# Optimization experiments

Hardware: AMD Instinct MI355X
Metric: run time of the kernel (lower is better)

The kernel has to match this reference:

```python
import jax, jax.numpy as jnp
import numpy as np

EMBED = 1152
HEADS = 16
HEAD_DIM = EMBED // HEADS
SCALE = HEAD_DIM ** -0.5


def setup_inputs() -> dict:
    key = jax.random.key(0)
    k1, k2, k3, k4, k5 = jax.random.split(key, 5)
    B, S = 32, 729
    std = EMBED ** -0.5
    return {
        "hidden_state": jax.random.normal(k1, (B, S, EMBED), dtype=jnp.float32),
        "qkv_w": jax.random.normal(k2, (3 * EMBED, EMBED), dtype=jnp.float32) * std,
        "qkv_b": jax.random.normal(k3, (3 * EMBED,), dtype=jnp.float32) * 0.02,
        "out_w": jax.random.normal(k4, (EMBED, EMBED), dtype=jnp.float32) * std,
        "out_b": jax.random.normal(k5, (EMBED,), dtype=jnp.float32) * 0.02,
    }


def reference(hidden_state, qkv_w, qkv_b, out_w, out_b):
    B, S, _ = hidden_state.shape
    qkv = hidden_state @ qkv_w.T + qkv_b  # [B,S,3E]
    q, k, v = jnp.split(qkv, 3, axis=-1)
    # [B,S,E] -> [B,H,S,Dh]
    def heads(x):
        return x.reshape(B, S, HEADS, HEAD_DIM).transpose(0, 2, 1, 3)
    q, k, v = heads(q), heads(k), heads(v)
    scores = jnp.einsum("bhqd,bhkd->bhqk", q, k) * SCALE
    scores = jax.nn.softmax(scores, axis=-1)  # [B,H,S,S]
    out = jnp.einsum("bhqk,bhkd->bhqd", scores, v)
    out = out.transpose(0, 2, 1, 3).reshape(B, S, EMBED)
    out = out @ out_w.T + out_b
    return out, scores
```

## Files before the change

### kernel.cpp

```cpp
#include <hip/hip_runtime.h>

#define B_    32
#define S_    729
#define E_    1152
#define H_    16
#define D_    72
#define M1_   23328
#define MPAD_ 23424
#define SQ_   736
#define SK_   768
#define DP_   96
#define VR_   96
#define SCALE_ 0.11785113019775793f

typedef __attribute__((ext_vector_type(8))) _Float16 f16x8;
typedef __attribute__((ext_vector_type(4))) _Float16 f16x4;
typedef __attribute__((ext_vector_type(4))) float    f32x4;

#define GLDS16(g, l) __builtin_amdgcn_global_load_lds(                      \
    (__attribute__((address_space(1))) void*)(g),                           \
    (__attribute__((address_space(3))) void*)(l), 16, 0, 0)

union H2U { _Float16 h[2]; uint32_t u; };

#define N4H  6718464
#define N4W1 995328
#define N4W2 331776
#define NQC  (512 * 736 * 3)
#define NKC  (512 * 768 * 3)
#define NVR  (512 * 72)
__global__ void cvt_all(const float* __restrict__ hid, const float* __restrict__ w1,
                        const float* __restrict__ w2, _Float16* __restrict__ o1,
                        _Float16* __restrict__ o2, _Float16* __restrict__ o3,
                        _Float16* __restrict__ Qp, _Float16* __restrict__ Kp,
                        _Float16* __restrict__ Vtp) {
  const int stride = gridDim.x * blockDim.x;
  const int tid0 = blockIdx.x * blockDim.x + threadIdx.x;
  const uint4 z4 = make_uint4(0, 0, 0, 0);
  for (int idx = tid0; idx < NQC; idx += stride) {
    int row = idx / 3, c = idx - row * 3;
    *(uint4*)((char*)Qp + (size_t)row * 192 + 144 + c * 16) = z4;
  }
  for (int idx = tid0; idx < NKC; idx += stride) {
    int row = idx / 3, c = idx - row * 3;
    *(uint4*)((char*)Kp + (size_t)row * 192 + 144 + c * 16) = z4;
  }
  for (int idx = tid0; idx < NVR; idx += stride) {
    _Float16* p = Vtp + (size_t)idx * 768 + 729;
    #pragma unroll
    for (int s = 0; s < 39; ++s) p[s] = (_Float16)0.0f;
  }
  for (int i = tid0; i < N4H + N4W1 + N4W2; i += stride) {
    const float* s; _Float16* d; int j;
    if (i < N4H)             { s = hid; d = o1; j = i; }
    else if (i < N4H + N4W1) { s = w1;  d = o2; j = i - N4H; }
    else                     { s = w2;  d = o3; j = i - N4H - N4W1; }
    f32x4 v = __builtin_nontemporal_load((const f32x4*)(s + (size_t)j * 4));
    f16x4 o;
    o[0] = (_Float16)v[0]; o[1] = (_Float16)v[1];
    o[2] = (_Float16)v[2]; o[3] = (_Float16)v[3];
    __builtin_nontemporal_store(o, (f16x4*)(d + (size_t)j * 4));
  }
}

template<int MODE>
__global__ __launch_bounds__(256)
void gemm_f16(const _Float16* __restrict__ A, const _Float16* __restrict__ W,
              const float* __restrict__ bias,
              _Float16* __restrict__ Qp, _Float16* __restrict__ Kp,
              _Float16* __restrict__ Vtp, float* __restrict__ Cout)
{
  int mb, nb;
  if (MODE == 0) {
    const int xcd  = blockIdx.x & 7;
    const int slot = blockIdx.x >> 3;
    const int st   = slot >> 4;
    const int w    = slot & 15;
    const int stm  = st % 6, stn = st / 6;
    const int mloc = stm * 4 + (w & 3);
    nb = stn * 4 + (w >> 2);
    const int stripe = (xcd < 7) ? 23 : 22;
    if (mloc >= stripe || nb >= 27) return;
    mb = (xcd < 7 ? xcd * 23 : 161) + mloc;
  } else {
    mb = blockIdx.x; nb = blockIdx.y;
  }

  __shared__ _Float16 As[128 * 64];
  __shared__ _Float16 Bs[128 * 64];
  const int tid = threadIdx.x;
  const int l  = tid & 63;
  const int wv = tid >> 6;
  const int lq = l & 15, lk = l >> 4;
  const int m0 = mb * 128;
  const int n0 = nb * 128;
  const int wm = (wv & 1) * 64, wn = (wv >> 1) * 64;
  const int srow = l >> 3;
  const int scol = (l & 7) * 8;

  f32x4 acc[4][4] = {};

  for (int k0 = 0; k0 < 1152; k0 += 64) {
    #pragma unroll
    for (int q = 0; q < 4; ++q) {
      int chunk = wv * 4 + q;
      int row = chunk * 8 + srow;
      GLDS16(A + (size_t)(m0 + row) * 1152 + k0 + scol, &As[chunk * 512 + l * 8]);
      GLDS16(W + (size_t)(n0 + row) * 1152 + k0 + scol, &Bs[chunk * 512 + l * 8]);
    }
    __syncthreads();
    #pragma unroll
    for (int kk = 0; kk < 64; kk += 32) {
      f16x8 a[4], b[4];
      #pragma unroll
      for (int i = 0; i < 4; ++i)
        a[i] = *(const f16x8*)&As[(wm + 16 * i + lq) * 64 + kk + lk * 8];
      #pragma unroll
      for (int j = 0; j < 4; ++j)
        b[j] = *(const f16x8*)&Bs[(wn + 16 * j + lq) * 64 + kk + lk * 8];
      #pragma unroll
      for (int i = 0; i < 4; ++i)
        #pragma unroll
        for (int j = 0; j < 4; ++j)
          acc[i][j] = __builtin_amdgcn_mfma_f32_16x16x32_f16(a[i], b[j], acc[i][j], 0, 0, 0);
    }
    __syncthreads();
  }

  #pragma unroll
  for (int i = 0; i < 4; ++i) {
    #pragma unroll
    for (int j = 0; j < 4; ++j) {
      int n = n0 + wn + 16 * j + lq;
      float bn = bias[n];
      #pragma unroll
      for (int r = 0; r < 4; ++r) {
        int m = m0 + wm + 16 * i + lk * 4 + r;
        if (m >= M1_) continue;
        float v = acc[i][j][r] + bn;
        if (MODE == 0) {
          unsigned um = (unsigned)m;
          unsigned bq = um / 729u, s = um - bq * 729u;
          unsigned un = (unsigned)n;
          unsigned which = un / 1152u, e = un - which * 1152u;
          unsigned h = e / 72u, d = e - h * 72u;
          unsigned bh = bq * 16u + h;
          if (which == 0) {
            Qp[((size_t)bh * SQ_ + s) * DP_ + d] = (_Float16)(v * SCALE_);
          } else if (which == 1) {
            Kp[((size_t)bh * SK_ + s) * DP_ + d] = (_Float16)v;
          } else {
            Vtp[((size_t)bh * VR_ + d) * 768 + s] = (_Float16)v;
          }
        } else {
          Cout[(size_t)m * 1152 + n] = v;
        }
      }
    }
  }
}

struct AttnSmem {
  union {
    char     stage[2][24576];
    float    ored[4][32][96];
    _Float16 p16[32][768];
  };
  uint32_t pexch[8][64][4];
  float redmax[32][4];
  float redsum[32][4];
  float invl[32];
};

__global__ __launch_bounds__(512, 4)
void attn_k(const _Float16* __restrict__ Q, const _Float16* __restrict__ K,
            const _Float16* __restrict__ Vt, float* __restrict__ scores,
            _Float16* __restrict__ AO)
{
  __shared__ AttnSmem sm;
  const int tid = threadIdx.x;
  const int l   = tid & 63;
  const int wv  = tid >> 6;
  const int lq  = l & 15, lk = l >> 4;
  const int i   = wv >> 2;
  const int sl  = wv & 3;
  const int p    = blockIdx.x;
  const int xcd  = p & 7;
  const int slot = p >> 3;
  const int hl   = slot / 23;
  const int qt   = slot - hl * 23;
  const int bh   = hl * 8 + xcd;
  const int q0   = qt * 32;
  const int b    = bh >> 4, h = bh & 15;

  const _Float16* Qb = Q  + (size_t)bh * SQ_ * DP_;
  const _Float16* Kb = K  + (size_t)bh * SK_ * DP_;
  const _Float16* Vb = Vt + (size_t)bh * VR_ * 768;

  auto stage = [&](int idx) {
    char* buf = sm.stage[idx & 1];
    if (idx < 6) {
      #pragma unroll
      for (int it = 0; it < 3; ++it) {
        int s = it * 512 + tid;
        int row = s / 12, cp = s - row * 12;
        int cc = (cp < 8) ? (cp ^ (row & 7)) : (8 + ((cp & 3) ^ ((row >> 1) & 3)));
        GLDS16(Kb + (size_t)(idx * 128 + row) * DP_ + cc * 8, buf + s * 16);
      }
    } else {
      #pragma unroll
      for (int it = 0; it < 3; ++it) {
        int s = it * 512 + tid;
        int row = s >> 4, cp = s & 15;
        int cc = cp ^ (row & 15);
        GLDS16(Vb + (size_t)row * 768 + (idx - 6) * 128 + cc * 8, buf + s * 16);
      }
    }
  };

  stage(0);
  stage(1);
  f16x8 aq[3];
  {
    const _Float16* qp = Qb + (size_t)(q0 + 16 * i + lq) * DP_ + lk * 8;
    aq[0] = *(const f16x8*)(qp);
    aq[1] = *(const f16x8*)(qp + 32);
    aq[2] = *(const f16x8*)(qp + 64);
  }
  asm volatile("s_waitcnt vmcnt(0)" ::: "memory");
  __builtin_amdgcn_s_barrier();

  f32x4 sacc[12] = {};
  #pragma unroll
  for (int t = 0; t < 6; ++t) {
    asm volatile("s_waitcnt vmcnt(3)" ::: "memory");
    __builtin_amdgcn_s_barrier();
    const char* bufp = sm.stage[t & 1];
    #pragma unroll
    for (int lcb = 0; lcb < 2; ++lcb) {
      int row = (2 * sl + lcb) * 16 + lq;
      #pragma unroll
      for (int t3 = 0; t3 < 3; ++t3) {
        int cc = 4 * t3 + lk;
        int cp = (cc < 8) ? (cc ^ (row & 7)) : (8 + ((cc & 3) ^ ((row >> 1) & 3)));
        f16x8 ka = *(const f16x8*)(bufp + row * 192 + cp * 16);
        sacc[2 * t + lcb] = __builtin_amdgcn_mfma_f32_16x16x32_f16(ka, aq[t3], sacc[2 * t + lcb], 0, 0, 0);
      }
    }
    asm volatile("s_waitcnt lgkmcnt(0)" ::: "memory");
    __builtin_amdgcn_s_barrier();
    stage(t + 2);
  }

  #pragma unroll
  for (int c = 10; c < 12; ++c) {
    int kbase = (40 + 2 * sl + (c & 1)) * 16 + 4 * lk;
    #pragma unroll
    for (int r = 0; r < 4; ++r)
      if (kbase + r > 728) sacc[c][r] = -1e30f;
  }

  float m = -1e30f;
  #pragma unroll
  for (int c = 0; c < 12; ++c)
    #pragma unroll
    for (int r = 0; r < 4; ++r) m = fmaxf(m, sacc[c][r]);
  m = fmaxf(m, __shfl_xor(m, 16));
  m = fmaxf(m, __shfl_xor(m, 32));
  if (lk == 0) sm.redmax[16 * i + lq][sl] = m;
  asm volatile("s_waitcnt lgkmcnt(0)" ::: "memory");
  __builtin_amdgcn_s_barrier();
  float gm;
  { const float* rp = sm.redmax[16 * i + lq];
    gm = fmaxf(fmaxf(rp[0], rp[1]), fmaxf(rp[2], rp[3])); }

  float sum = 0.f;
  #pragma unroll
  for (int c = 0; c < 12; ++c)
    #pragma unroll
    for (int r = 0; r < 4; ++r) {
      float e = __expf(sacc[c][r] - gm);
      sacc[c][r] = e;
      sum += e;
    }
  sum += __shfl_xor(sum, 16);
  sum += __shfl_xor(sum, 32);
  if (lk == 0) sm.redsum[16 * i + lq][sl] = sum;
  asm volatile("s_waitcnt lgkmcnt(0)" ::: "memory");
  __builtin_amdgcn_s_barrier();
  float inv;
  { const float* rp = sm.redsum[16 * i + lq];
    inv = 1.0f / (rp[0] + rp[1] + rp[2] + rp[3]); }
  if (lk == 0 && sl == 0) sm.invl[16 * i + lq] = inv;

  uint32_t pk[12][2];
  #pragma unroll
  for (int c = 0; c < 12; ++c) {
    H2U a0, a1;
    a0.h[0] = (_Float16)sacc[c][0]; a0.h[1] = (_Float16)sacc[c][1];
    a1.h[0] = (_Float16)sacc[c][2]; a1.h[1] = (_Float16)sacc[c][3];
    pk[c][0] = a0.u; pk[c][1] = a1.u;
  }

  f32x4 oacc[6] = {};
  const int srcA = lq + 16 * (2 * (lk & 1));
  const int srcB = srcA + 16;
  #pragma unroll
  for (int v = 0; v < 6; ++v) {
    if (v < 5) { asm volatile("s_waitcnt vmcnt(3)" ::: "memory"); }
    else       { asm volatile("s_waitcnt vmcnt(0)" ::: "memory"); }
    __builtin_amdgcn_s_barrier();
    uint4 w = make_uint4(pk[2 * v][0], pk[2 * v][1], pk[2 * v + 1][0], pk[2 * v + 1][1]);
    *(uint4*)&sm.pexch[wv][l][0] = w;
    asm volatile("s_waitcnt lgkmcnt(0)" ::: "memory");
    __builtin_amdgcn_sched_barrier(0);
    uint2 dA = *(const uint2*)((const char*)&sm.pexch[wv][srcA][0] + (lk >> 1) * 8);
    uint2 dB = *(const uint2*)((const char*)&sm.pexch[wv][srcB][0] + (lk >> 1) * 8);
    uint4 pad4 = make_uint4(dA.x, dA.y, dB.x, dB.y);
    f16x8 pa = __builtin_bit_cast(f16x8, pad4);

    const char* bufp = sm.stage[v & 1];
    #pragma unroll
    for (int db = 0; db < 6; ++db) {
      int row = db * 16 + lq;
      int cc = 4 * sl + lk;
      int cp = cc ^ (row & 15);
      f16x8 bv = *(const f16x8*)(bufp + row * 256 + cp * 16);
      oacc[db] = __builtin_amdgcn_mfma_f32_16x16x32_f16(pa, bv, oacc[db], 0, 0, 0);
    }
    asm volatile("s_waitcnt lgkmcnt(0)" ::: "memory");
    __builtin_amdgcn_s_barrier();
    if (v < 4) stage(v + 8);
  }

  #pragma unroll
  for (int db = 0; db < 6; ++db)
    #pragma unroll
    for (int r = 0; r < 4; ++r) {
      int row = 16 * i + lk * 4 + r;
      sm.ored[sl][row][(db * 16 + lq) ^ (row & 12)] = oacc[db][r];
    }
  asm volatile("s_waitcnt lgkmcnt(0)" ::: "memory");
  __builtin_amdgcn_s_barrier();

  {
    int qq = tid >> 4, dc = tid & 15;
    int qglob = q0 + qq;
    if (dc < 12 && qglob < S_) {
      int d0 = dc * 6;
      float iv = sm.invl[qq];
      _Float16* ap = AO + ((size_t)(b * S_ + qglob)) * E_ + h * D_ + d0;
      #pragma unroll
      for (int e = 0; e < 6; ++e) {
        int col = (d0 + e) ^ (qq & 12);
        float v = sm.ored[0][qq][col] + sm.ored[1][qq][col]
                + sm.ored[2][qq][col] + sm.ored[3][qq][col];
        ap[e] = (_Float16)(v * iv);
      }
    }
  }
  asm volatile("s_waitcnt lgkmcnt(0)" ::: "memory");
  __builtin_amdgcn_s_barrier();

  {
    int row = 16 * i + lq;
    char* base = (char*)sm.p16 + row * 1536;
    #pragma unroll
    for (int c = 0; c < 12; ++c) {
      int cb = 8 * (c >> 1) + 2 * sl + (c & 1);
      int off = cb * 32 + 8 * lk;
      int swz = off ^ ((row & 7) << 4);
      *(uint2*)(base + swz) = make_uint2(pk[c][0], pk[c][1]);
    }
  }
  asm volatile("s_waitcnt lgkmcnt(0)" ::: "memory");
  __builtin_amdgcn_s_barrier();

  {
    #pragma unroll
    for (int rr = 0; rr < 4; ++rr) {
      int row = wv * 4 + rr;
      int qg  = q0 + row;
      if (qg < S_) {
        float ivr = sm.invl[row];
        float* srow = scores + (size_t)bh * S_ * S_ + (size_t)qg * S_;
        const char* base = (const char*)sm.p16 + row * 1536;
        #pragma unroll
        for (int u = 0; u < 3; ++u) {
          int off = u * 512 + 8 * l;
          int swz = off ^ ((row & 7) << 4);
          f16x4 pv4 = *(const f16x4*)(base + swz);
          int k0 = u * 256 + 4 * l;
          f32x4 vv;
          vv[0] = (float)pv4[0] * ivr; vv[1] = (float)pv4[1] * ivr;
          vv[2] = (float)pv4[2] * ivr; vv[3] = (float)pv4[3] * ivr;
          if (k0 + 3 <= 728)
            __builtin_nontemporal_store(vv, (f32x4*)(srow + k0));
          else if (k0 == 728)
            __builtin_nontemporal_store(vv[0], srow + 728);
        }
      }
    }
  }
}

extern "C" void kernel_launch(void* const* d_in, const int* in_sizes, int n_in,
                              void* d_out, int out_size, void* d_ws, size_t ws_size,
                              hipStream_t stream)
{
  const float* hidden = (const float*)d_in[0];
  const float* qkv_w  = (const float*)d_in[1];
  const float* qkv_b  = (const float*)d_in[2];
  const float* out_w  = (const float*)d_in[3];
  const float* out_b  = (const float*)d_in[4];
  float* out    = (float*)d_out;
  float* scores = out + (size_t)M1_ * E_;

  char* ws = (char*)d_ws;
  const size_t szA1 = (size_t)MPAD_ * 1152 * 2;
  const size_t szWq = (size_t)3456 * 1152 * 2;
  const size_t szWo = (size_t)1152 * 1152 * 2;
  const size_t szQ  = (size_t)512 * SQ_ * DP_ * 2;
  const size_t szK  = (size_t)512 * SK_ * DP_ * 2;
  const size_t szV  = (size_t)512 * VR_ * 768 * 2;
  const size_t offA1 = 0;
  const size_t offWq = offA1 + szA1;
  const size_t offWo = offWq + szWq;
  const size_t offQ  = offWo + szWo;
  const size_t offK  = offQ  + szQ;
  const size_t offVt = offK  + szK;
  const size_t need  = offVt + szV;
  if (ws_size < need) return;

  _Float16* A1  = (_Float16*)(ws + offA1);
  _Float16* Wq  = (_Float16*)(ws + offWq);
  _Float16* Wo  = (_Float16*)(ws + offWo);
  _Float16* Qp  = (_Float16*)(ws + offQ);
  _Float16* Kp  = (_Float16*)(ws + offK);
  _Float16* Vtp = (_Float16*)(ws + offVt);
  _Float16* AO  = A1;

  cvt_all<<<2048, 256, 0, stream>>>(hidden, qkv_w, out_w, A1, Wq, Wo, Qp, Kp, Vtp);

  gemm_f16<0><<<5376, 256, 0, stream>>>(A1, Wq, qkv_b, Qp, Kp, Vtp, nullptr);
  attn_k<<<11776, 512, 0, stream>>>(Qp, Kp, Vtp, scores, AO);
  gemm_f16<1><<<dim3(183, 9), 256, 0, stream>>>(AO, Wo, out_b, nullptr, nullptr, nullptr, out);
}
```

Measured before the change: 1.109 ms.

## Double attention query tile to 64 rows to halve K/V staging per query

Each attention block now processes 64 query rows instead of 32, with the 8 waves split into 4 query groups by 2 key slices instead of 2 by 4. K and V tiles staged into LDS are reused across twice as many queries, halving global K/V traffic and block count. The cost is doubled per-thread score and packed-probability registers (24 accumulators), which may cut occupancy or cause spills, plus a two-pass score writeout through LDS. Q padding grows to 768 rows.

```diff
diff --git a/kernel.cpp b/kernel.cpp
--- a/kernel.cpp
+++ b/kernel.cpp
@@ -7,7 +7,7 @@
 #define D_    72
 #define M1_   23328
 #define MPAD_ 23424
-#define SQ_   736
+#define SQ_   768
 #define SK_   768
 #define DP_   96
 #define VR_   96
@@ -26,7 +26,7 @@
 #define N4H  6718464
 #define N4W1 995328
 #define N4W2 331776
-#define NQC  (512 * 736 * 3)
+#define NQC  (512 * 768 * 3)
 #define NKC  (512 * 768 * 3)
 #define NVR  (512 * 72)
 __global__ void cvt_all(const float* __restrict__ hid, const float* __restrict__ w1,
@@ -163,13 +163,13 @@
 struct AttnSmem {
   union {
     char     stage[2][24576];
-    float    ored[4][32][96];
+    float    ored[2][64][96];
     _Float16 p16[32][768];
   };
   uint32_t pexch[8][64][4];
-  float redmax[32][4];
-  float redsum[32][4];
-  float invl[32];
+  float redmax[64][2];
+  float redsum[64][2];
+  float invl[64];
 };
 
 __global__ __launch_bounds__(512, 4)
@@ -182,15 +182,15 @@
   const int l   = tid & 63;
   const int wv  = tid >> 6;
   const int lq  = l & 15, lk = l >> 4;
-  const int i   = wv >> 2;
-  const int sl  = wv & 3;
+  const int i   = wv >> 1;
+  const int sl  = wv & 1;
   const int p    = blockIdx.x;
   const int xcd  = p & 7;
   const int slot = p >> 3;
-  const int hl   = slot / 23;
-  const int qt   = slot - hl * 23;
+  const int hl   = slot / 12;
+  const int qt   = slot - hl * 12;
   const int bh   = hl * 8 + xcd;
-  const int q0   = qt * 32;
+  const int q0   = qt * 64;
   const int b    = bh >> 4, h = bh & 15;
 
   const _Float16* Qb = Q  + (size_t)bh * SQ_ * DP_;
@@ -230,21 +230,23 @@
   asm volatile("s_waitcnt vmcnt(0)" ::: "memory");
   __builtin_amdgcn_s_barrier();
 
-  f32x4 sacc[12] = {};
+  f32x4 sacc[24] = {};
   #pragma unroll
   for (int t = 0; t < 6; ++t) {
     asm volatile("s_waitcnt vmcnt(3)" ::: "memory");
     __builtin_amdgcn_s_barrier();
     const char* bufp = sm.stage[t & 1];
     #pragma unroll
-    for (int lcb = 0; lcb < 2; ++lcb) {
-      int row = (2 * sl + lcb) * 16 + lq;
+    for (int j = 0; j < 4; ++j) {
+      int c = 4 * t + j;
+      int lcb = 4 * (j >> 1) + 2 * sl + (j & 1);
+      int row = lcb * 16 + lq;
       #pragma unroll
       for (int t3 = 0; t3 < 3; ++t3) {
         int cc = 4 * t3 + lk;
         int cp = (cc < 8) ? (cc ^ (row & 7)) : (8 + ((cc & 3) ^ ((row >> 1) & 3)));
         f16x8 ka = *(const f16x8*)(bufp + row * 192 + cp * 16);
-        sacc[2 * t + lcb] = __builtin_amdgcn_mfma_f32_16x16x32_f16(ka, aq[t3], sacc[2 * t + lcb], 0, 0, 0);
+        sacc[c] = __builtin_amdgcn_mfma_f32_16x16x32_f16(ka, aq[t3], sacc[c], 0, 0, 0);
       }
     }
     asm volatile("s_waitcnt lgkmcnt(0)" ::: "memory");
@@ -252,17 +254,18 @@
     stage(t + 2);
   }
 
-  #pragma unroll
-  for (int c = 10; c < 12; ++c) {
-    int kbase = (40 + 2 * sl + (c & 1)) * 16 + 4 * lk;
+  if (sl == 0) {
     #pragma unroll
     for (int r = 0; r < 4; ++r)
-      if (kbase + r > 728) sacc[c][r] = -1e30f;
+      if (720 + 4 * lk + r > 728) sacc[23][r] = -1e30f;
+  } else {
+    #pragma unroll
+    for (int r = 0; r < 4; ++r) { sacc[22][r] = -1e30f; sacc[23][r] = -1e30f; }
   }
 
   float m = -1e30f;
   #pragma unroll
-  for (int c = 0; c < 12; ++c)
+  for (int c = 0; c < 24; ++c)
     #pragma unroll
     for (int r = 0; r < 4; ++r) m = fmaxf(m, sacc[c][r]);
   m = fmaxf(m, __shfl_xor(m, 16));
@@ -272,11 +275,11 @@
   __builtin_amdgcn_s_barrier();
   float gm;
   { const float* rp = sm.redmax[16 * i + lq];
-    gm = fmaxf(fmaxf(rp[0], rp[1]), fmaxf(rp[2], rp[3])); }
+    gm = fmaxf(rp[0], rp[1]); }
 
   float sum = 0.f;
   #pragma unroll
-  for (int c = 0; c < 12; ++c)
+  for (int c = 0; c < 24; ++c)
     #pragma unroll
     for (int r = 0; r < 4; ++r) {
       float e = __expf(sacc[c][r] - gm);
@@ -290,12 +293,12 @@
   __builtin_amdgcn_s_barrier();
   float inv;
   { const float* rp = sm.redsum[16 * i + lq];
-    inv = 1.0f / (rp[0] + rp[1] + rp[2] + rp[3]); }
+    inv = 1.0f / (rp[0] + rp[1]); }
   if (lk == 0 && sl == 0) sm.invl[16 * i + lq] = inv;
 
-  uint32_t pk[12][2];
-  #pragma unroll
-  for (int c = 0; c < 12; ++c) {
+  uint32_t pk[24][2];
+  #pragma unroll
+  for (int c = 0; c < 24; ++c) {
     H2U a0, a1;
     a0.h[0] = (_Float16)sacc[c][0]; a0.h[1] = (_Float16)sacc[c][1];
     a1.h[0] = (_Float16)sacc[c][2]; a1.h[1] = (_Float16)sacc[c][3];
@@ -310,23 +313,40 @@
     if (v < 5) { asm volatile("s_waitcnt vmcnt(3)" ::: "memory"); }
     else       { asm volatile("s_waitcnt vmcnt(0)" ::: "memory"); }
     __builtin_amdgcn_s_barrier();
-    uint4 w = make_uint4(pk[2 * v][0], pk[2 * v][1], pk[2 * v + 1][0], pk[2 * v + 1][1]);
-    *(uint4*)&sm.pexch[wv][l][0] = w;
+    f16x8 pa0, pa1;
+    {
+      uint4 w = make_uint4(pk[4 * v][0], pk[4 * v][1], pk[4 * v + 1][0], pk[4 * v + 1][1]);
+      *(uint4*)&sm.pexch[wv][l][0] = w;
+      asm volatile("s_waitcnt lgkmcnt(0)" ::: "memory");
+      __builtin_amdgcn_sched_barrier(0);
+      uint2 dA = *(const uint2*)((const char*)&sm.pexch[wv][srcA][0] + (lk >> 1) * 8);
+      uint2 dB = *(const uint2*)((const char*)&sm.pexch[wv][srcB][0] + (lk >> 1) * 8);
+      pa0 = __builtin_bit_cast(f16x8, make_uint4(dA.x, dA.y, dB.x, dB.y));
+    }
     asm volatile("s_waitcnt lgkmcnt(0)" ::: "memory");
     __builtin_amdgcn_sched_barrier(0);
-    uint2 dA = *(const uint2*)((const char*)&sm.pexch[wv][srcA][0] + (lk >> 1) * 8);
-    uint2 dB = *(const uint2*)((const char*)&sm.pexch[wv][srcB][0] + (lk >> 1) * 8);
-    uint4 pad4 = make_uint4(dA.x, dA.y, dB.x, dB.y);
-    f16x8 pa = __builtin_bit_cast(f16x8, pad4);
+    {
+      uint4 w = make_uint4(pk[4 * v + 2][0], pk[4 * v + 2][1], pk[4 * v + 3][0], pk[4 * v + 3][1]);
+      *(uint4*)&sm.pexch[wv][l][0] = w;
+      asm volatile("s_waitcnt lgkmcnt(0)" ::: "memory");
+      __builtin_amdgcn_sched_barrier(0);
+      uint2 dA = *(const uint2*)((const char*)&sm.pexch[wv][srcA][0] + (lk >> 1) * 8);
+      uint2 dB = *(const uint2*)((const char*)&sm.pexch[wv][srcB][0] + (lk >> 1) * 8);
+      pa1 = __builtin_bit_cast(f16x8, make_uint4(dA.x, dA.y, dB.x, dB.y));
+    }
 
     const char* bufp = sm.stage[v & 1];
     #pragma unroll
     for (int db = 0; db < 6; ++db) {
       int row = db * 16 + lq;
-      int cc = 4 * sl + lk;
-      int cp = cc ^ (row & 15);
-      f16x8 bv = *(const f16x8*)(bufp + row * 256 + cp * 16);
-      oacc[db] = __builtin_amdgcn_mfma_f32_16x16x32_f16(pa, bv, oacc[db], 0, 0, 0);
+      int cc0 = 4 * sl + lk;
+      int cp0 = cc0 ^ (row & 15);
+      f16x8 bv0 = *(const f16x8*)(bufp + row * 256 + cp0 * 16);
+      oacc[db] = __builtin_amdgcn_mfma_f32_16x16x32_f16(pa0, bv0, oacc[db], 0, 0, 0);
+      int cc1 = 8 + 4 * sl + lk;
+      int cp1 = cc1 ^ (row & 15);
+      f16x8 bv1 = *(const f16x8*)(bufp + row * 256 + cp1 * 16);
+      oacc[db] = __builtin_amdgcn_mfma_f32_16x16x32_f16(pa1, bv1, oacc[db], 0, 0, 0);
     }
     asm volatile("s_waitcnt lgkmcnt(0)" ::: "memory");
     __builtin_amdgcn_s_barrier();
@@ -344,17 +364,16 @@
   __builtin_amdgcn_s_barrier();
 
   {
-    int qq = tid >> 4, dc = tid & 15;
+    int qq = tid >> 3, dc = tid & 7;
     int qglob = q0 + qq;
-    if (dc < 12 && qglob < S_) {
-      int d0 = dc * 6;
+    if (qglob < S_) {
+      int d0 = dc * 9;
       float iv = sm.invl[qq];
       _Float16* ap = AO + ((size_t)(b * S_ + qglob)) * E_ + h * D_ + d0;
       #pragma unroll
-      for (int e = 0; e < 6; ++e) {
+      for (int e = 0; e < 9; ++e) {
         int col = (d0 + e) ^ (qq & 12);
-        float v = sm.ored[0][qq][col] + sm.ored[1][qq][col]
-                + sm.ored[2][qq][col] + sm.ored[3][qq][col];
+        float v = sm.ored[0][qq][col] + sm.ored[1][qq][col];
         ap[e] = (_Float16)(v * iv);
       }
     }
@@ -362,33 +381,35 @@
   asm volatile("s_waitcnt lgkmcnt(0)" ::: "memory");
   __builtin_amdgcn_s_barrier();
 
-  {
-    int row = 16 * i + lq;
-    char* base = (char*)sm.p16 + row * 1536;
-    #pragma unroll
-    for (int c = 0; c < 12; ++c) {
-      int cb = 8 * (c >> 1) + 2 * sl + (c & 1);
-      int off = cb * 32 + 8 * lk;
-      int swz = off ^ ((row & 7) << 4);
-      *(uint2*)(base + swz) = make_uint2(pk[c][0], pk[c][1]);
-    }
-  }
-  asm volatile("s_waitcnt lgkmcnt(0)" ::: "memory");
-  __builtin_amdgcn_s_barrier();
-
-  {
+  #pragma unroll
+  for (int pass = 0; pass < 2; ++pass) {
+    if ((i >> 1) == pass) {
+      int lrow = 16 * (i & 1) + lq;
+      char* base = (char*)sm.p16 + lrow * 1536;
+      #pragma unroll
+      for (int c = 0; c < 24; ++c) {
+        int cb = 4 * (c >> 1) + 2 * sl + (c & 1);
+        int off = cb * 32 + 8 * lk;
+        int swz = off ^ ((lrow & 7) << 4);
+        *(uint2*)(base + swz) = make_uint2(pk[c][0], pk[c][1]);
+      }
+    }
+    asm volatile("s_waitcnt lgkmcnt(0)" ::: "memory");
+    __builtin_amdgcn_s_barrier();
+
     #pragma unroll
     for (int rr = 0; rr < 4; ++rr) {
-      int row = wv * 4 + rr;
-      int qg  = q0 + row;
+      int lrow = wv * 4 + rr;
+      int grow = 32 * pass + lrow;
+      int qg   = q0 + grow;
       if (qg < S_) {
-        float ivr = sm.invl[row];
+        float ivr = sm.invl[grow];
         float* srow = scores + (size_t)bh * S_ * S_ + (size_t)qg * S_;
-        const char* base = (const char*)sm.p16 + row * 1536;
+        const char* base = (const char*)sm.p16 + lrow * 1536;
         #pragma unroll
         for (int u = 0; u < 3; ++u) {
           int off = u * 512 + 8 * l;
-          int swz = off ^ ((row & 7) << 4);
+          int swz = off ^ ((lrow & 7) << 4);
           f16x4 pv4 = *(const f16x4*)(base + swz);
           int k0 = u * 256 + 4 * l;
           f32x4 vv;
@@ -400,6 +421,10 @@
             __builtin_nontemporal_store(vv[0], srow + 728);
         }
       }
+    }
+    if (pass == 0) {
+      asm volatile("s_waitcnt lgkmcnt(0)" ::: "memory");
+      __builtin_amdgcn_s_barrier();
     }
   }
 }
@@ -443,6 +468,6 @@
   cvt_all<<<2048, 256, 0, stream>>>(hidden, qkv_w, out_w, A1, Wq, Wo, Qp, Kp, Vtp);
 
   gemm_f16<0><<<5376, 256, 0, stream>>>(A1, Wq, qkv_b, Qp, Kp, Vtp, nullptr);
-  attn_k<<<11776, 512, 0, stream>>>(Qp, Kp, Vtp, scores, AO);
+  attn_k<<<6144, 512, 0, stream>>>(Qp, Kp, Vtp, scores, AO);
   gemm_f16<1><<<dim3(183, 9), 256, 0, stream>>>(AO, Wo, out_b, nullptr, nullptr, nullptr, out);
 }
```

Measured after the change: 1.196 ms. +7.8%, slower.
